# Kernel tuning notes

Measured on AMD Instinct MI355X. Metric: run time of the kernel, lower is better.

Reference implementation:

```python
import jax, jax.numpy as jnp
import numpy as np

N = 200000          # active sites
H = W_GRID = 1024   # dense grid extent
CIN = 256           # inplanes * 4
CMID = 64           # inplanes
KVOL = 9            # 3x3 kernel volume


def setup_inputs() -> dict:
    rng = np.random.default_rng(0)
    # unique active coordinates on the grid
    flat = rng.choice(H * W_GRID, size=N, replace=False)
    ys = (flat // W_GRID).astype(np.int64)
    xs = (flat % W_GRID).astype(np.int64)
    # dense hash: grid[y,x] = site index, -1 if inactive (padded border)
    grid = np.full((H + 2, W_GRID + 2), -1, dtype=np.int32)
    grid[ys + 1, xs + 1] = np.arange(N, dtype=np.int32)
    offsets = [(dy, dx) for dy in (-1, 0, 1) for dx in (-1, 0, 1)]
    # rulebook: for each active site, index of each 3x3 neighbor (-1 if inactive)
    nbr = np.stack([grid[ys + 1 + dy, xs + 1 + dx] for dy, dx in offsets], axis=1)  # [N, 9]

    key = jax.random.key(0)
    k1, k2, k3, k4 = jax.random.split(key, 4)
    features = jax.random.normal(k1, (N, CIN), dtype=jnp.float32)
    # scn conv weights: [kernel_volume, Cin, Cout], no bias
    W1 = jax.random.normal(k2, (CIN, CMID), dtype=jnp.float32) * (1.0 / np.sqrt(CIN))
    W2 = jax.random.normal(k3, (KVOL, CMID, CMID), dtype=jnp.float32) * (1.0 / np.sqrt(KVOL * CMID))
    W3 = jax.random.normal(k4, (CMID, CIN), dtype=jnp.float32) * (1.0 / np.sqrt(CMID))
    return {"features": features, "W1": W1, "W2": W2, "W3": W3,
            "neighbor_idx": jnp.asarray(nbr)}


def subm_conv3x3(x, W2, neighbor_idx):
    # gather active neighbors (rulebook), zero inactive ones, per-offset GEMM, scatter-sum
    mask = (neighbor_idx >= 0)                                  # [N, 9]
    gathered = x[jnp.maximum(neighbor_idx, 0)] * mask[..., None].astype(x.dtype)  # [N, 9, Cmid]
    return jnp.einsum('nkc,kcd->nd', gathered, W2)              # [N, Cmid]


def reference(features, W1, W2, W3, neighbor_idx):
    residual = features
    out = jax.nn.relu(features @ W1)                 # conv1 (1x1 subm) + relu
    out = jax.nn.relu(subm_conv3x3(out, W2, neighbor_idx))  # conv2 (3x3 subm) + relu
    out = out @ W3                                   # conv3 (1x1 subm)
    return jax.nn.relu(out + residual)               # add + relu
```

## Files before the change

### kernel.cpp

```cpp
#include <hip/hip_runtime.h>
#include <hip/hip_bf16.h>

#define N_SITES 200000
#define CIN 256
#define CMID 64
#define KVOL 9

using bf16x8 = __attribute__((ext_vector_type(8))) short;
using f32x4  = __attribute__((ext_vector_type(4))) float;

__device__ __forceinline__ short f2bf(float f) {
    union { float f; unsigned u; } v; v.f = f;
    unsigned r = v.u + 0x7fffu + ((v.u >> 16) & 1u);
    return (short)(r >> 16);
}

__device__ __forceinline__ f32x4 mfma16(bf16x8 a, bf16x8 b, f32x4 c) {
    return __builtin_amdgcn_mfma_f32_16x16x32_bf16(a, b, c, 0, 0, 0);
}

__global__ __launch_bounds__(256) void k1_conv1(const float* __restrict__ feat,
                                                const float* __restrict__ W1,
                                                const float* __restrict__ W2,
                                                const float* __restrict__ W3,
                                                short* __restrict__ x1,
                                                short* __restrict__ W2T,
                                                short* __restrict__ W3T) {
    const int t = threadIdx.x;
    const int gt = blockIdx.x * 256 + t;
    if (gt < KVOL * CMID * CMID) {
        int kk = gt >> 12, rem = gt & 4095, co = rem >> 6, k = rem & 63;
        W2T[gt] = f2bf(W2[kk * 4096 + k * 64 + co]);
    }
    if (gt < CMID * CIN) {
        int co = gt >> 6, k = gt & 63;
        W3T[gt] = f2bf(W3[k * 256 + co]);
    }

    __shared__ short w1t[64][264];
    __shared__ short o1[64][72];
    const int lane = t & 63, w = t >> 6;
    const int r = lane & 15, g = lane >> 4;

    #pragma unroll
    for (int qq = 0; qq < 16; ++qq) {
        int k0 = 4 * w + 16 * qq;
        float v0 = W1[(k0 + 0) * 64 + lane];
        float v1 = W1[(k0 + 1) * 64 + lane];
        float v2 = W1[(k0 + 2) * 64 + lane];
        float v3 = W1[(k0 + 3) * 64 + lane];
        *(short4*)&w1t[lane][k0] = make_short4(f2bf(v0), f2bf(v1), f2bf(v2), f2bf(v3));
    }
    __syncthreads();

    const int row0 = blockIdx.x * 64 + w * 16;
    const float* ap = feat + (size_t)(row0 + r) * CIN + g * 8;

    f32x4 acc[4] = {};
    #pragma unroll
    for (int ks = 0; ks < 8; ++ks) {
        f32x4 a0 = *(const f32x4*)(ap + ks * 32);
        f32x4 a1 = *(const f32x4*)(ap + ks * 32 + 4);
        bf16x8 af;
        #pragma unroll
        for (int j = 0; j < 4; ++j) { af[j] = f2bf(a0[j]); af[4 + j] = f2bf(a1[j]); }
        #pragma unroll
        for (int ct = 0; ct < 4; ++ct) {
            bf16x8 bf = *(const bf16x8*)&w1t[ct * 16 + r][ks * 32 + g * 8];
            acc[ct] = mfma16(af, bf, acc[ct]);
        }
    }
    #pragma unroll
    for (int ct = 0; ct < 4; ++ct)
        #pragma unroll
        for (int j = 0; j < 4; ++j) {
            float v = acc[ct][j];
            o1[w * 16 + g * 4 + j][ct * 16 + r] = f2bf(v > 0.f ? v : 0.f);
        }
    __syncthreads();
    #pragma unroll
    for (int i = 0; i < 2; ++i) {
        int v = t + 256 * i; int row = v >> 3, c8 = v & 7;
        *(bf16x8*)&x1[(size_t)(blockIdx.x * 64 + row) * CMID + c8 * 8] =
            *(const bf16x8*)&o1[row][c8 * 8];
    }
}

__global__ __launch_bounds__(256) void k23_fused(const short* __restrict__ x1,
                                                 const short* __restrict__ W2T,
                                                 const short* __restrict__ W3T,
                                                 const int* __restrict__ nbr,
                                                 const float* __restrict__ feat,
                                                 float* __restrict__ out) {
    __shared__ short w2t[2][64][72];
    __shared__ short w3t[128][72];
    auto ot = reinterpret_cast<float(*)[16][36]>(&w2t[0][0][0]);
    auto o2 = reinterpret_cast<short(*)[16][72]>(&w3t[0][0]);

    const int t = threadIdx.x;
    const int lane = t & 63, w = t >> 6;
    const int r = lane & 15, g = lane >> 4;

    const int nwg = gridDim.x;
    const int q = nwg >> 3, rm = nwg & 7;
    const int xcd = blockIdx.x & 7, pos = blockIdx.x >> 3;
    const int bid = (xcd < rm) ? xcd * (q + 1) + pos
                               : rm * (q + 1) + (xcd - rm) * q + pos;

    const int row0 = bid * 64 + w * 16;
    const int site = row0 + r;

    int idx9[9];
    #pragma unroll
    for (int kk = 0; kk < 9; ++kk) idx9[kk] = nbr[site * 9 + kk];

    {
        const short* src = W2T + t * 8;
        bf16x8 v0 = *(const bf16x8*)(src);
        bf16x8 v1 = *(const bf16x8*)(src + 2048);
        *(bf16x8*)&w2t[0][(t >> 3)][(t & 7) * 8] = v0;
        *(bf16x8*)&w2t[0][(t >> 3) + 32][(t & 7) * 8] = v1;
    }
    bf16x8 ga[3], gb[3];
    #pragma unroll
    for (int p = 0; p < 3; ++p) {
        ga[p] = (bf16x8){}; gb[p] = (bf16x8){};
        int ii = idx9[p];
        if (ii >= 0) { const short* gp = x1 + (size_t)ii * CMID + g * 8;
                       ga[p] = *(const bf16x8*)gp; gb[p] = *(const bf16x8*)(gp + 32); }
    }
    __syncthreads();

    f32x4 acc2[4] = {};
    #pragma unroll
    for (int kk = 0; kk < 9; ++kk) {
        const int cur = kk % 3;
        bf16x8 a0 = ga[cur], a1 = gb[cur];
        bf16x8 n0 = {}, n1 = {};
        if (kk + 3 < 9) {
            int ii = idx9[kk + 3];
            if (ii >= 0) { const short* gp = x1 + (size_t)ii * CMID + g * 8;
                           n0 = *(const bf16x8*)gp; n1 = *(const bf16x8*)(gp + 32); }
        }
        ga[cur] = n0; gb[cur] = n1;
        bf16x8 s0, s1;
        if (kk < 8) {
            const short* src = W2T + (kk + 1) * 4096 + t * 8;
            s0 = *(const bf16x8*)(src);
            s1 = *(const bf16x8*)(src + 2048);
        }
        #pragma unroll
        for (int ct = 0; ct < 4; ++ct) {
            bf16x8 b0 = *(const bf16x8*)&w2t[kk & 1][ct * 16 + r][g * 8];
            bf16x8 b1 = *(const bf16x8*)&w2t[kk & 1][ct * 16 + r][32 + g * 8];
            acc2[ct] = mfma16(a0, b0, acc2[ct]);
            acc2[ct] = mfma16(a1, b1, acc2[ct]);
        }
        if (kk < 8) {
            *(bf16x8*)&w2t[(kk & 1) ^ 1][(t >> 3)][(t & 7) * 8] = s0;
            *(bf16x8*)&w2t[(kk & 1) ^ 1][(t >> 3) + 32][(t & 7) * 8] = s1;
        }
        __syncthreads();
    }

    #pragma unroll
    for (int ct = 0; ct < 4; ++ct)
        #pragma unroll
        for (int j = 0; j < 4; ++j) {
            float v = acc2[ct][j];
            o2[w][g * 4 + j][ct * 16 + r] = f2bf(v > 0.f ? v : 0.f);
        }
    asm volatile("s_waitcnt lgkmcnt(0)" ::: "memory");
    bf16x8 A0 = *(const bf16x8*)&o2[w][r][g * 8];
    bf16x8 A1 = *(const bf16x8*)&o2[w][r][32 + g * 8];

    #pragma unroll
    for (int h = 0; h < 2; ++h) {
        __syncthreads();
        {
            const short* src = W3T + h * 8192 + t * 8;
            #pragma unroll
            for (int i = 0; i < 4; ++i) {
                bf16x8 u = *(const bf16x8*)(src + i * 2048);
                *(bf16x8*)&w3t[(t >> 3) + i * 32][(t & 7) * 8] = u;
            }
        }
        __syncthreads();

        f32x4 acc3[8];
        #pragma unroll
        for (int ct = 0; ct < 8; ++ct) {
            bf16x8 b0 = *(const bf16x8*)&w3t[ct * 16 + r][g * 8];
            bf16x8 b1 = *(const bf16x8*)&w3t[ct * 16 + r][32 + g * 8];
            f32x4 z = {};
            z = mfma16(A0, b0, z);
            acc3[ct] = mfma16(A1, b1, z);
        }

        #pragma unroll
        for (int c = 0; c < 4; ++c) {
            #pragma unroll
            for (int ci = 0; ci < 2; ++ci)
                #pragma unroll
                for (int j = 0; j < 4; ++j)
                    ot[w][g * 4 + j][ci * 16 + r] = acc3[c * 2 + ci][j];
            asm volatile("s_waitcnt lgkmcnt(0)" ::: "memory");
            #pragma unroll
            for (int i = 0; i < 2; ++i) {
                int v = lane + 64 * i;
                int row = v >> 3, c4 = v & 7;
                size_t o = (size_t)(row0 + row) * CIN + h * 128 + c * 32 + c4 * 4;
                f32x4 f = *(const f32x4*)&feat[o];
                f32x4 s = *(const f32x4*)&ot[w][row][c4 * 4];
                f32x4 res;
                #pragma unroll
                for (int j = 0; j < 4; ++j) { float x = s[j] + f[j]; res[j] = x > 0.f ? x : 0.f; }
                __builtin_nontemporal_store(res, (f32x4*)&out[o]);
            }
        }
    }
}

extern "C" void kernel_launch(void* const* d_in, const int* in_sizes, int n_in,
                              void* d_out, int out_size, void* d_ws, size_t ws_size,
                              hipStream_t stream) {
    const float* feat = (const float*)d_in[0];
    const float* W1   = (const float*)d_in[1];
    const float* W2   = (const float*)d_in[2];
    const float* W3   = (const float*)d_in[3];
    const int*   nbr  = (const int*)d_in[4];

    short* x1  = (short*)d_ws;
    short* W2T = x1 + (size_t)N_SITES * CMID;
    short* W3T = W2T + KVOL * CMID * CMID;
    float* out = (float*)d_out;

    const int blocks = N_SITES / 64;
    hipLaunchKernelGGL(k1_conv1, dim3(blocks), dim3(256), 0, stream,
                       feat, W1, W2, W3, x1, W2T, W3T);
    hipLaunchKernelGGL(k23_fused, dim3(blocks), dim3(256), 0, stream,
                       x1, W2T, W3T, nbr, feat, out);
}
```

Before: 121.2 us.

## Make conv2+conv3 kernel persistent with all weights resident in LDS

Replaces the per-64-row fused conv2/conv3 kernel with a persistent kernel of 256 blocks of 512 threads. Each block loads all nine W2 taps and the full W3 into shared memory once, then each wave independently loops over 16-site units with no block-level barriers. The goal is to stop reloading weights and double-buffering W2 per tile, and to remove the per-tap syncthreads. The cost is a large LDS footprint (about 124 KB) that allows only one block per CU, a fixed static split of units with some tail imbalance, and deeper gather prefetch that raises register pressure.

```diff
diff --git a/kernel.cpp b/kernel.cpp
--- a/kernel.cpp
+++ b/kernel.cpp
@@ -5,6 +5,7 @@
 #define CIN 256
 #define CMID 64
 #define KVOL 9
+#define UNITS 12500
 
 using bf16x8 = __attribute__((ext_vector_type(8))) short;
 using f32x4  = __attribute__((ext_vector_type(4))) float;
@@ -86,110 +87,89 @@
     }
 }
 
-__global__ __launch_bounds__(256) void k23_fused(const short* __restrict__ x1,
-                                                 const short* __restrict__ W2T,
-                                                 const short* __restrict__ W3T,
-                                                 const int* __restrict__ nbr,
-                                                 const float* __restrict__ feat,
-                                                 float* __restrict__ out) {
-    __shared__ short w2t[2][64][72];
-    __shared__ short w3t[128][72];
-    auto ot = reinterpret_cast<float(*)[16][36]>(&w2t[0][0][0]);
-    auto o2 = reinterpret_cast<short(*)[16][72]>(&w3t[0][0]);
+__global__ __launch_bounds__(512) void k23_persist(const short* __restrict__ x1,
+                                                   const short* __restrict__ W2T,
+                                                   const short* __restrict__ W3T,
+                                                   const int* __restrict__ nbr,
+                                                   const float* __restrict__ feat,
+                                                   float* __restrict__ out) {
+    __shared__ short w2t[9][64][72];
+    __shared__ short w3t[256][72];
+    __shared__ short sc[8][16][72];
 
     const int t = threadIdx.x;
-    const int lane = t & 63, w = t >> 6;
+    const int lane = t & 63, wv = t >> 6;
     const int r = lane & 15, g = lane >> 4;
 
-    const int nwg = gridDim.x;
-    const int q = nwg >> 3, rm = nwg & 7;
-    const int xcd = blockIdx.x & 7, pos = blockIdx.x >> 3;
-    const int bid = (xcd < rm) ? xcd * (q + 1) + pos
-                               : rm * (q + 1) + (xcd - rm) * q + pos;
-
-    const int row0 = bid * 64 + w * 16;
-    const int site = row0 + r;
-
-    int idx9[9];
-    #pragma unroll
-    for (int kk = 0; kk < 9; ++kk) idx9[kk] = nbr[site * 9 + kk];
-
-    {
-        const short* src = W2T + t * 8;
-        bf16x8 v0 = *(const bf16x8*)(src);
-        bf16x8 v1 = *(const bf16x8*)(src + 2048);
-        *(bf16x8*)&w2t[0][(t >> 3)][(t & 7) * 8] = v0;
-        *(bf16x8*)&w2t[0][(t >> 3) + 32][(t & 7) * 8] = v1;
-    }
-    bf16x8 ga[3], gb[3];
-    #pragma unroll
-    for (int p = 0; p < 3; ++p) {
-        ga[p] = (bf16x8){}; gb[p] = (bf16x8){};
-        int ii = idx9[p];
-        if (ii >= 0) { const short* gp = x1 + (size_t)ii * CMID + g * 8;
-                       ga[p] = *(const bf16x8*)gp; gb[p] = *(const bf16x8*)(gp + 32); }
+    #pragma unroll
+    for (int kk = 0; kk < 9; ++kk) {
+        bf16x8 v = *(const bf16x8*)(W2T + kk * 4096 + t * 8);
+        *(bf16x8*)&w2t[kk][t >> 3][(t & 7) * 8] = v;
+    }
+    #pragma unroll
+    for (int i = 0; i < 4; ++i) {
+        bf16x8 v = *(const bf16x8*)(W3T + i * 4096 + t * 8);
+        *(bf16x8*)&w3t[i * 64 + (t >> 3)][(t & 7) * 8] = v;
     }
     __syncthreads();
 
-    f32x4 acc2[4] = {};
-    #pragma unroll
-    for (int kk = 0; kk < 9; ++kk) {
-        const int cur = kk % 3;
-        bf16x8 a0 = ga[cur], a1 = gb[cur];
-        bf16x8 n0 = {}, n1 = {};
-        if (kk + 3 < 9) {
-            int ii = idx9[kk + 3];
+    auto ot = reinterpret_cast<float(*)[36]>(&sc[wv][0][0]);
+
+    const int ustart = blockIdx.x * 49;
+    const int uend = (ustart + 49 < UNITS) ? ustart + 49 : UNITS;
+    for (int u = ustart + wv; u < uend; u += 8) {
+        const int site0 = u * 16;
+        const int site = site0 + r;
+
+        int idx9[9];
+        #pragma unroll
+        for (int kk = 0; kk < 9; ++kk) idx9[kk] = nbr[site * 9 + kk];
+
+        bf16x8 ga[4], gb[4];
+        #pragma unroll
+        for (int p = 0; p < 4; ++p) {
+            ga[p] = (bf16x8){}; gb[p] = (bf16x8){};
+            int ii = idx9[p];
             if (ii >= 0) { const short* gp = x1 + (size_t)ii * CMID + g * 8;
-                           n0 = *(const bf16x8*)gp; n1 = *(const bf16x8*)(gp + 32); }
-        }
-        ga[cur] = n0; gb[cur] = n1;
-        bf16x8 s0, s1;
-        if (kk < 8) {
-            const short* src = W2T + (kk + 1) * 4096 + t * 8;
-            s0 = *(const bf16x8*)(src);
-            s1 = *(const bf16x8*)(src + 2048);
-        }
-        #pragma unroll
-        for (int ct = 0; ct < 4; ++ct) {
-            bf16x8 b0 = *(const bf16x8*)&w2t[kk & 1][ct * 16 + r][g * 8];
-            bf16x8 b1 = *(const bf16x8*)&w2t[kk & 1][ct * 16 + r][32 + g * 8];
-            acc2[ct] = mfma16(a0, b0, acc2[ct]);
-            acc2[ct] = mfma16(a1, b1, acc2[ct]);
-        }
-        if (kk < 8) {
-            *(bf16x8*)&w2t[(kk & 1) ^ 1][(t >> 3)][(t & 7) * 8] = s0;
-            *(bf16x8*)&w2t[(kk & 1) ^ 1][(t >> 3) + 32][(t & 7) * 8] = s1;
-        }
-        __syncthreads();
-    }
-
-    #pragma unroll
-    for (int ct = 0; ct < 4; ++ct)
-        #pragma unroll
-        for (int j = 0; j < 4; ++j) {
-            float v = acc2[ct][j];
-            o2[w][g * 4 + j][ct * 16 + r] = f2bf(v > 0.f ? v : 0.f);
-        }
-    asm volatile("s_waitcnt lgkmcnt(0)" ::: "memory");
-    bf16x8 A0 = *(const bf16x8*)&o2[w][r][g * 8];
-    bf16x8 A1 = *(const bf16x8*)&o2[w][r][32 + g * 8];
-
-    #pragma unroll
-    for (int h = 0; h < 2; ++h) {
-        __syncthreads();
-        {
-            const short* src = W3T + h * 8192 + t * 8;
-            #pragma unroll
-            for (int i = 0; i < 4; ++i) {
-                bf16x8 u = *(const bf16x8*)(src + i * 2048);
-                *(bf16x8*)&w3t[(t >> 3) + i * 32][(t & 7) * 8] = u;
-            }
-        }
-        __syncthreads();
-
-        f32x4 acc3[8];
-        #pragma unroll
-        for (int ct = 0; ct < 8; ++ct) {
+                           ga[p] = *(const bf16x8*)gp; gb[p] = *(const bf16x8*)(gp + 32); }
+        }
+
+        f32x4 acc2[4] = {};
+        #pragma unroll
+        for (int kk = 0; kk < 9; ++kk) {
+            const int cur = kk & 3;
+            bf16x8 a0 = ga[cur], a1 = gb[cur];
+            if (kk + 4 < 9) {
+                int ii = idx9[kk + 4];
+                bf16x8 n0 = {}, n1 = {};
+                if (ii >= 0) { const short* gp = x1 + (size_t)ii * CMID + g * 8;
+                               n0 = *(const bf16x8*)gp; n1 = *(const bf16x8*)(gp + 32); }
+                ga[cur] = n0; gb[cur] = n1;
+            }
+            #pragma unroll
+            for (int ct = 0; ct < 4; ++ct) {
+                bf16x8 b0 = *(const bf16x8*)&w2t[kk][ct * 16 + r][g * 8];
+                bf16x8 b1 = *(const bf16x8*)&w2t[kk][ct * 16 + r][32 + g * 8];
+                acc2[ct] = mfma16(a0, b0, acc2[ct]);
+                acc2[ct] = mfma16(a1, b1, acc2[ct]);
+            }
+        }
+
+        #pragma unroll
+        for (int ct = 0; ct < 4; ++ct)
+            #pragma unroll
+            for (int j = 0; j < 4; ++j) {
+                float v = acc2[ct][j];
+                sc[wv][g * 4 + j][ct * 16 + r] = f2bf(v > 0.f ? v : 0.f);
+            }
+        asm volatile("s_waitcnt lgkmcnt(0)" ::: "memory");
+        bf16x8 A0 = *(const bf16x8*)&sc[wv][r][g * 8];
+        bf16x8 A1 = *(const bf16x8*)&sc[wv][r][32 + g * 8];
+        asm volatile("s_waitcnt lgkmcnt(0)" ::: "memory");
+
+        f32x4 acc3[16];
+        #pragma unroll
+        for (int ct = 0; ct < 16; ++ct) {
             bf16x8 b0 = *(const bf16x8*)&w3t[ct * 16 + r][g * 8];
             bf16x8 b1 = *(const bf16x8*)&w3t[ct * 16 + r][32 + g * 8];
             f32x4 z = {};
@@ -198,20 +178,20 @@
         }
 
         #pragma unroll
-        for (int c = 0; c < 4; ++c) {
+        for (int c = 0; c < 8; ++c) {
             #pragma unroll
             for (int ci = 0; ci < 2; ++ci)
                 #pragma unroll
                 for (int j = 0; j < 4; ++j)
-                    ot[w][g * 4 + j][ci * 16 + r] = acc3[c * 2 + ci][j];
+                    ot[g * 4 + j][ci * 16 + r] = acc3[c * 2 + ci][j];
             asm volatile("s_waitcnt lgkmcnt(0)" ::: "memory");
             #pragma unroll
             for (int i = 0; i < 2; ++i) {
                 int v = lane + 64 * i;
                 int row = v >> 3, c4 = v & 7;
-                size_t o = (size_t)(row0 + row) * CIN + h * 128 + c * 32 + c4 * 4;
+                size_t o = (size_t)(site0 + row) * CIN + c * 32 + c4 * 4;
                 f32x4 f = *(const f32x4*)&feat[o];
-                f32x4 s = *(const f32x4*)&ot[w][row][c4 * 4];
+                f32x4 s = *(const f32x4*)&ot[row][c4 * 4];
                 f32x4 res;
                 #pragma unroll
                 for (int j = 0; j < 4; ++j) { float x = s[j] + f[j]; res[j] = x > 0.f ? x : 0.f; }
@@ -238,6 +218,6 @@
     const int blocks = N_SITES / 64;
     hipLaunchKernelGGL(k1_conv1, dim3(blocks), dim3(256), 0, stream,
                        feat, W1, W2, W3, x1, W2T, W3T);
-    hipLaunchKernelGGL(k23_fused, dim3(blocks), dim3(256), 0, stream,
+    hipLaunchKernelGGL(k23_persist, dim3(256), dim3(512), 0, stream,
                        x1, W2T, W3T, nbr, feat, out);
 }
```

Result: no change. 120.5 us (-0.6%).
